# Optimization experiments

Hardware: AMD Instinct MI355X
Metric: run time of the kernel (lower is better)

## Reference

```python
import jax, jax.numpy as jnp
import numpy as np

N_MODEL = 10000
N_DATA = 552
DIST_SCALE = 1.0e5  # scales uniform [0,1) to realistic squared distances (meters^2)


def setup_inputs() -> dict:
    key = jax.random.key(0)
    k0, k1, k2 = jax.random.split(key, 3)
    distance_mesh = jax.random.uniform(k0, (N_MODEL, N_MODEL), dtype=jnp.float32) * DIST_SCALE
    F = jax.random.normal(k1, (N_DATA, N_MODEL), dtype=jnp.float32) * 0.01
    d_obs = jax.random.normal(k2, (N_DATA, 1), dtype=jnp.float32)
    data_std = 0.1
    data_cov = (data_std ** 2) * jnp.eye(N_DATA, dtype=jnp.float32)
    m0 = jnp.asarray(2200.0, dtype=jnp.float32)
    length_scale = jnp.asarray(100.0, dtype=jnp.float32)
    sigma = jnp.asarray(20.0, dtype=jnp.float32)
    return {
        "distance_mesh": distance_mesh,
        "F": F,
        "d_obs": d_obs,
        "data_cov": data_cov,
        "m0": m0,
        "length_scale": length_scale,
        "sigma": sigma,
    }


def reference(distance_mesh, F, d_obs, data_cov, m0, length_scale, sigma):
    n_model = distance_mesh.shape[0]
    # m_prior = m0 * ones([n_model, 1])
    m_prior = m0 * jnp.ones((n_model, 1), dtype=distance_mesh.dtype)
    # Squared-exponential covariance: sigma^2 * exp(-d / (2 l^2))  [n_model, n_model]
    K = jnp.exp(distance_mesh * (-1.0 / (2.0 * length_scale ** 2))) * (sigma ** 2)
    # pushforward covariance K @ F.T  [n_model, n_data]
    pushforward_cov = K @ F.T
    # data-space operator [n_data, n_data]
    inv_inversion_operator = data_cov + F @ pushforward_cov
    inversion_operator = jnp.linalg.inv(inv_inversion_operator)
    log_det = -jnp.linalg.slogdet(inversion_operator)[1]
    prior_misfit = d_obs - F @ m_prior  # [n_data, 1]
    tmp = inversion_operator @ prior_misfit  # [n_data, 1]
    m_posterior = m_prior + pushforward_cov @ tmp  # [n_model, 1]
    log_likelyhood = log_det + prior_misfit.T @ tmp  # [1, 1]
    return (log_likelyhood, m_posterior)
```

## Files before the change

kernel.cpp:

```cpp
#include <hip/hip_runtime.h>
#include <stdint.h>


#define NM 10000
#define ND 552
#define NDP 576
#define NKB 313
#define MT1 79
#define SPLITK 3
#define SPLITK2 6

typedef __attribute__((ext_vector_type(8))) short bf16x8;
typedef __attribute__((ext_vector_type(4))) float f32x4;

__device__ __forceinline__ unsigned short f2bf(float f){
  unsigned u = __float_as_uint(f);
  u += 0x7fffu + ((u >> 16) & 1u);
  return (unsigned short)(u >> 16);
}
__device__ __forceinline__ unsigned int pk2(unsigned short a, unsigned short b){
  return (unsigned int)a | ((unsigned int)b << 16);
}

__global__ void prep_bt(const float* __restrict__ F, unsigned short* __restrict__ Bt){
  int bid = blockIdx.x;
  int kb = bid % NKB, nb = bid / NKB;
  int t = threadIdx.x;
  int nl = t >> 2, q = t & 3;
  int gn = nb * 64 + nl;
  int k0 = kb * 32 + q * 8;
  float v[8];
  if (gn < ND && (k0 + 8) <= NM){
    const float* p = F + (size_t)gn * NM + k0;
    float4 a = *(const float4*)p;
    float4 b = *(const float4*)(p + 4);
    v[0]=a.x; v[1]=a.y; v[2]=a.z; v[3]=a.w; v[4]=b.x; v[5]=b.y; v[6]=b.z; v[7]=b.w;
  } else {
    #pragma unroll
    for (int i = 0; i < 8; ++i) v[i] = 0.f;
  }
  unsigned short u[8];
  #pragma unroll
  for (int i = 0; i < 8; ++i) u[i] = f2bf(v[i]);
  size_t cidx = ((size_t)kb * NDP + gn) * 4 + ((q + (gn >> 1)) & 3);
  uint4 w;
  w.x = pk2(u[0],u[1]); w.y = pk2(u[2],u[3]); w.z = pk2(u[4],u[5]); w.w = pk2(u[6],u[7]);
  *(uint4*)(Bt + cidx * 8) = w;
}

__global__ void rvec(const float* __restrict__ F, const float* __restrict__ dobs,
                     const float* __restrict__ m0p, float* __restrict__ r){
  __shared__ float red[256];
  int i = blockIdx.x;
  int t = threadIdx.x;
  float s = 0.f;
  if (i < ND){
    for (int k = t; k < NM; k += 256) s += F[(size_t)i * NM + k];
  }
  red[t] = s;
  __syncthreads();
  if (t < 64){
    float v = red[t] + red[t+64] + red[t+128] + red[t+192];
    #pragma unroll
    for (int off = 32; off; off >>= 1) v += __shfl_down(v, off);
    if (t == 0){
      if (i < ND) r[i] = dobs[i] - m0p[0] * v;
      else        r[i] = 0.f;
    }
  }
}

__global__ __launch_bounds__(512, 2) void gemm1(
    const float* __restrict__ dist, const unsigned short* __restrict__ Bt,
    float* __restrict__ P, const float* __restrict__ lsp, const float* __restrict__ sgp){
  __shared__ unsigned short Alds[2][128 * 40];
  __shared__ unsigned short Blds[2][NDP * 32];
  int bid = blockIdx.x;
  int mtile = bid % MT1, kc = bid / MT1;
  int kb0 = (kc == 0) ? 0 : (105 + 104 * (kc - 1));
  int kbe = kb0 + ((kc == 0) ? 105 : 104);
  int m0 = mtile * 128;
  float ls = lsp[0], sg = sgp[0];
  float ce = -0.72134752044f / (ls * ls);
  float s2 = sg * sg;
  int t = threadIdx.x, lane = t & 63, w = t >> 6;
  int wm = w & 1, wn = w >> 1;
  int c16 = lane & 15, q2 = lane >> 4;
  f32x4 acc[4][9];
  #pragma unroll
  for (int a = 0; a < 4; ++a)
    #pragma unroll
    for (int b = 0; b < 9; ++b) acc[a][b] = (f32x4){0.f, 0.f, 0.f, 0.f};

  int rr = t >> 2, qa = t & 3;
  const int arow = (wm * 64 + c16) * 40 + q2 * 8;
  int gm = m0 + rr;
  const float* arow_p = dist + (size_t)gm * NM;

  float av[8];
  uint4 bv[4];
  uint4 btl;
  bool aok = false;

#define G1_ISSUE(KB) { \
    int k0_ = (KB) * 32 + qa * 8; \
    aok = (gm < NM) && (k0_ + 8 <= NM); \
    if (aok){ \
      const float4* p_ = (const float4*)(arow_p + k0_); \
      float4 x_ = p_[0]; float4 y_ = p_[1]; \
      av[0]=x_.x; av[1]=x_.y; av[2]=x_.z; av[3]=x_.w; \
      av[4]=y_.x; av[5]=y_.y; av[6]=y_.z; av[7]=y_.w; \
    } \
    const uint4* bs_ = (const uint4*)Bt + (size_t)(KB) * NDP * 4; \
    bv[0] = bs_[t]; bv[1] = bs_[t + 512]; bv[2] = bs_[t + 1024]; bv[3] = bs_[t + 1536]; \
    if (t < 256) btl = bs_[t + 2048]; \
  }

#define G1_STORE(BUF) { \
    unsigned short u_[8]; \
    if (aok){ \
      _Pragma("unroll") \
      for (int i_ = 0; i_ < 8; ++i_) u_[i_] = f2bf(s2 * exp2f(av[i_] * ce)); \
    } else { \
      _Pragma("unroll") \
      for (int i_ = 0; i_ < 8; ++i_) u_[i_] = 0; \
    } \
    uint4 wv_; \
    wv_.x = pk2(u_[0],u_[1]); wv_.y = pk2(u_[2],u_[3]); \
    wv_.z = pk2(u_[4],u_[5]); wv_.w = pk2(u_[6],u_[7]); \
    *(uint4*)&Alds[BUF][rr * 40 + qa * 8] = wv_; \
    uint4* bd_ = (uint4*)Blds[BUF]; \
    bd_[t] = bv[0]; bd_[t + 512] = bv[1]; bd_[t + 1024] = bv[2]; bd_[t + 1536] = bv[3]; \
    if (t < 256) bd_[t + 2048] = btl; \
  }

  G1_ISSUE(kb0);
  G1_STORE(0);
  __syncthreads();

  for (int kb = kb0; kb < kbe; ++kb){
    int cur = (kb - kb0) & 1;
    if (kb + 1 < kbe) G1_ISSUE(kb + 1);
    bf16x8 af[4];
    #pragma unroll
    for (int mt = 0; mt < 4; ++mt)
      af[mt] = *(const bf16x8*)&Alds[cur][arow + mt * 16 * 40];
    #pragma unroll
    for (int nt = 0; nt < 9; ++nt){
      int n = wn * 144 + nt * 16 + c16;
      int cidx = n * 4 + ((q2 + (n >> 1)) & 3);
      bf16x8 bfv = *(const bf16x8*)&Blds[cur][cidx * 8];
      #pragma unroll
      for (int mt = 0; mt < 4; ++mt)
        acc[mt][nt] = __builtin_amdgcn_mfma_f32_16x16x32_bf16(af[mt], bfv, acc[mt][nt], 0, 0, 0);
    }
    if (kb + 1 < kbe) G1_STORE(cur ^ 1);
    __syncthreads();
  }
#undef G1_ISSUE
#undef G1_STORE

  #pragma unroll
  for (int mt = 0; mt < 4; ++mt)
    #pragma unroll
    for (int nt = 0; nt < 9; ++nt)
      #pragma unroll
      for (int e = 0; e < 4; ++e){
        int gmo = m0 + wm * 64 + mt * 16 + q2 * 4 + e;
        int gno = wn * 144 + nt * 16 + c16;
        if (gmo < NM) atomicAdd(&P[(size_t)gmo * NDP + gno], acc[mt][nt][e]);
      }
}

__global__ void conv_p(const float* __restrict__ P, unsigned short* __restrict__ Pb){
  int bid = blockIdx.x;
  int kb = bid % NKB, nb = bid / NKB;
  int t = threadIdx.x;
  int nl = t & 63, q = t >> 6;
  int gn = nb * 64 + nl;
  int k0 = kb * 32 + q * 8;
  unsigned short u[8];
  #pragma unroll
  for (int j = 0; j < 8; ++j){
    int k = k0 + j;
    float v = (k < NM) ? P[(size_t)k * NDP + gn] : 0.f;
    u[j] = f2bf(v);
  }
  size_t cidx = ((size_t)kb * NDP + gn) * 4 + ((q + (gn >> 1)) & 3);
  uint4 w;
  w.x = pk2(u[0],u[1]); w.y = pk2(u[2],u[3]); w.z = pk2(u[4],u[5]); w.w = pk2(u[6],u[7]);
  *(uint4*)(Pb + cidx * 8) = w;
}

__global__ void a_init(const float* __restrict__ dcov, float* __restrict__ A){
  int idx = blockIdx.x * 256 + threadIdx.x;
  if (idx >= NDP * NDP) return;
  int i = idx / NDP, j = idx % NDP;
  float v;
  if (i < ND && j < ND) v = dcov[i * ND + j];
  else v = (i == j) ? 1.f : 0.f;
  A[idx] = v;
}

__global__ __launch_bounds__(256) void gemm2(
    const unsigned short* __restrict__ Bt, const unsigned short* __restrict__ Pb,
    float* __restrict__ A){
  __shared__ unsigned short Fa[2][64 * 32];
  __shared__ unsigned short Pl[2][64 * 32];
  int bid = blockIdx.x;
  int tile = bid % 81, kc = bid / 81;
  int ti = tile / 9, tj = tile % 9;
  int i0 = ti * 64, j0 = tj * 64;
  int kb0 = (kc == 0) ? 0 : (53 + 52 * (kc - 1));
  int kbe = kb0 + ((kc == 0) ? 53 : 52);
  int t = threadIdx.x, lane = t & 63, w = t >> 6;
  int wm = w & 1, wn = w >> 1;
  int c16 = lane & 15, q2 = lane >> 4;
  f32x4 acc[2][2];
  #pragma unroll
  for (int a = 0; a < 2; ++a)
    #pragma unroll
    for (int b = 0; b < 2; ++b) acc[a][b] = (f32x4){0.f, 0.f, 0.f, 0.f};

  uint4 fv, pv;
  fv = ((const uint4*)Bt)[((size_t)kb0 * NDP + i0) * 4 + t];
  pv = ((const uint4*)Pb)[((size_t)kb0 * NDP + j0) * 4 + t];
  ((uint4*)Fa[0])[t] = fv;
  ((uint4*)Pl[0])[t] = pv;
  __syncthreads();

  for (int kb = kb0; kb < kbe; ++kb){
    int cur = (kb - kb0) & 1;
    if (kb + 1 < kbe){
      fv = ((const uint4*)Bt)[((size_t)(kb + 1) * NDP + i0) * 4 + t];
      pv = ((const uint4*)Pb)[((size_t)(kb + 1) * NDP + j0) * 4 + t];
    }
    bf16x8 af[2], bfv[2];
    #pragma unroll
    for (int mt = 0; mt < 2; ++mt){
      int il = wm * 32 + mt * 16 + c16;
      af[mt] = *(const bf16x8*)&Fa[cur][(il * 4 + ((q2 + (il >> 1)) & 3)) * 8];
    }
    #pragma unroll
    for (int nt = 0; nt < 2; ++nt){
      int jl = wn * 32 + nt * 16 + c16;
      bfv[nt] = *(const bf16x8*)&Pl[cur][(jl * 4 + ((q2 + (jl >> 1)) & 3)) * 8];
    }
    #pragma unroll
    for (int mt = 0; mt < 2; ++mt)
      #pragma unroll
      for (int nt = 0; nt < 2; ++nt)
        acc[mt][nt] = __builtin_amdgcn_mfma_f32_16x16x32_bf16(af[mt], bfv[nt], acc[mt][nt], 0, 0, 0);
    if (kb + 1 < kbe){
      ((uint4*)Fa[cur ^ 1])[t] = fv;
      ((uint4*)Pl[cur ^ 1])[t] = pv;
    }
    __syncthreads();
  }
  #pragma unroll
  for (int mt = 0; mt < 2; ++mt)
    #pragma unroll
    for (int nt = 0; nt < 2; ++nt)
      #pragma unroll
      for (int e = 0; e < 4; ++e){
        int gi = i0 + wm * 32 + mt * 16 + q2 * 4 + e;
        int gj = j0 + wn * 32 + nt * 16 + c16;
        atomicAdd(&A[(size_t)gi * NDP + gj], acc[mt][nt][e]);
      }
}

__global__ __launch_bounds__(256) void lu_trsm(float* __restrict__ A,
                                               float* __restrict__ D, int k0){
  __shared__ float Dg[64 * 65];
  __shared__ float Tg[64 * 65];
  int t = threadIdx.x;
  int nch = (NDP - k0 - 64) >> 6;
  int bid = blockIdx.x;
  bool writer = (bid == 2 * nch);
  bool isU = bid < nch;
  int ch = isU ? bid : bid - nch;
  int c0 = k0 + 64 + ch * 64;
  int rbase = isU ? k0 : c0;
  int cbase = isU ? c0 : k0;
  for (int fid = t; fid < 1024; fid += 256){
    int row = fid >> 4, c4 = (fid & 15) << 2;
    float4 v = *(const float4*)&A[(size_t)(k0 + row) * NDP + k0 + c4];
    Dg[row * 65 + c4 + 0] = v.x; Dg[row * 65 + c4 + 1] = v.y;
    Dg[row * 65 + c4 + 2] = v.z; Dg[row * 65 + c4 + 3] = v.w;
  }
  if (!writer){
    for (int fid = t; fid < 1024; fid += 256){
      int row = fid >> 4, c4 = (fid & 15) << 2;
      float4 v = *(const float4*)&A[(size_t)(rbase + row) * NDP + cbase + c4];
      Tg[row * 65 + c4 + 0] = v.x; Tg[row * 65 + c4 + 1] = v.y;
      Tg[row * 65 + c4 + 2] = v.z; Tg[row * 65 + c4 + 3] = v.w;
    }
  }
  __syncthreads();
  if (t < 64){
    int l = t;
    float rg[64];
    #pragma unroll
    for (int c = 0; c < 64; ++c) rg[c] = Dg[l * 65 + c];
    #pragma unroll
    for (int j = 0; j < 64; ++j){
      float piv = __shfl(rg[j], j);
      float lij = rg[j] / piv;
      float m = (l > j) ? 1.f : 0.f;
      float mlij = m * lij;
      #pragma unroll
      for (int c = j + 1; c < 64; ++c){
        float rjc = __shfl(rg[c], j);
        rg[c] -= mlij * rjc;
      }
      if (l > j) rg[j] = lij;
    }
    #pragma unroll
    for (int c = 0; c < 64; ++c) Dg[l * 65 + c] = rg[c];
  }
  __syncthreads();
  if (writer){
    float* dd = D + (size_t)(k0 >> 6) * 4096;
    for (int fid = t; fid < 1024; fid += 256){
      int row = fid >> 4, c4 = (fid & 15) << 2;
      float4 v;
      v.x = Dg[row * 65 + c4 + 0]; v.y = Dg[row * 65 + c4 + 1];
      v.z = Dg[row * 65 + c4 + 2]; v.w = Dg[row * 65 + c4 + 3];
      *(float4*)&dd[row * 64 + c4] = v;
    }
    return;
  }
  if (t < 64){
    if (isU){
      float x[64];
      #pragma unroll
      for (int i = 0; i < 64; ++i) x[i] = Tg[i * 65 + t];
      #pragma unroll
      for (int i = 0; i < 64; ++i){
        #pragma unroll
        for (int ii = i + 1; ii < 64; ++ii)
          x[ii] -= Dg[ii * 65 + i] * x[i];
      }
      #pragma unroll
      for (int i = 0; i < 64; ++i) Tg[i * 65 + t] = x[i];
    } else {
      float x[64];
      #pragma unroll
      for (int j = 0; j < 64; ++j) x[j] = Tg[t * 65 + j];
      #pragma unroll
      for (int j = 0; j < 64; ++j){
        x[j] /= Dg[j * 65 + j];
        #pragma unroll
        for (int jj = j + 1; jj < 64; ++jj)
          x[jj] -= x[j] * Dg[j * 65 + jj];
      }
      #pragma unroll
      for (int j = 0; j < 64; ++j) Tg[t * 65 + j] = x[j];
    }
  }
  __syncthreads();
  for (int fid = t; fid < 1024; fid += 256){
    int row = fid >> 4, c4 = (fid & 15) << 2;
    float4 v;
    v.x = Tg[row * 65 + c4 + 0]; v.y = Tg[row * 65 + c4 + 1];
    v.z = Tg[row * 65 + c4 + 2]; v.w = Tg[row * 65 + c4 + 3];
    *(float4*)&A[(size_t)(rbase + row) * NDP + cbase + c4] = v;
  }
}

__global__ __launch_bounds__(256) void lu_gemmk(float* __restrict__ A, int k0){
  __shared__ float Lt[32 * 65];
  __shared__ float Ut[64 * 33];
  int n2 = NDP - k0 - 64;
  int nb = n2 >> 5;
  int bx = blockIdx.x % nb, by = blockIdx.x / nb;
  int r0 = k0 + 64 + bx * 32, c0 = k0 + 64 + by * 32;
  int t = threadIdx.x;
  for (int idx = t; idx < 2048; idx += 256){
    int i = idx >> 6, kk = idx & 63;
    Lt[i * 65 + kk] = A[(size_t)(r0 + i) * NDP + k0 + kk];
  }
  for (int idx = t; idx < 2048; idx += 256){
    int kk = idx >> 5, j = idx & 31;
    Ut[kk * 33 + j] = A[(size_t)(k0 + kk) * NDP + c0 + j];
  }
  __syncthreads();
  int i = t >> 3, j4 = (t & 7) * 4;
  float acc[4] = {0.f, 0.f, 0.f, 0.f};
  for (int kk = 0; kk < 64; ++kk){
    float lv = Lt[i * 65 + kk];
    #pragma unroll
    for (int u = 0; u < 4; ++u) acc[u] += lv * Ut[kk * 33 + j4 + u];
  }
  float* dst = &A[(size_t)(r0 + i) * NDP + c0 + j4];
  #pragma unroll
  for (int u = 0; u < 4; ++u) dst[u] -= acc[u];
}

__global__ __launch_bounds__(576) void solve_ll(
    const float* __restrict__ A, const float* __restrict__ D,
    const float* __restrict__ r, float* __restrict__ tmp, float* __restrict__ out0){
  __shared__ float ys[NDP];
  __shared__ float red[16];
  int t = threadIdx.x;
  int w = t >> 6, l = t & 63;
  int i = t;
  float y = r[i];
  float rsave = y;
  float ldpart = 0.f;
  float row[64];

  for (int jb = 0; jb < 9; ++jb){
    if (w == jb){
      const float4* ap = (const float4*)(D + (size_t)jb * 4096 + (size_t)l * 64);
      #pragma unroll
      for (int q = 0; q < 16; ++q) ((float4*)row)[q] = ap[q];
    } else if (w > jb){
      const float4* ap = (const float4*)(A + (size_t)i * NDP + jb * 64);
      #pragma unroll
      for (int q = 0; q < 16; ++q) ((float4*)row)[q] = ap[q];
    }
    if (w == jb){
      #pragma unroll
      for (int j = 0; j < 64; ++j){
        float yj = __shfl(y, j);
        if (l > j) y -= row[j] * yj;
      }
      ys[i] = y;
    }
    __syncthreads();
    if (w > jb){
      #pragma unroll
      for (int j = 0; j < 64; ++j) y -= row[j] * ys[jb * 64 + j];
    }
  }
  __syncthreads();

  for (int jb = 8; jb >= 0; --jb){
    if (w == jb){
      const float4* ap = (const float4*)(D + (size_t)jb * 4096 + (size_t)l * 64);
      #pragma unroll
      for (int q = 0; q < 16; ++q) ((float4*)row)[q] = ap[q];
    } else if (w < jb){
      const float4* ap = (const float4*)(A + (size_t)i * NDP + jb * 64);
      #pragma unroll
      for (int q = 0; q < 16; ++q) ((float4*)row)[q] = ap[q];
    }
    if (w == jb){
      float dv = D[(size_t)jb * 4096 + (size_t)l * 64 + l];
      float dinv = 1.f / dv;
      ldpart = logf(fabsf(dv));
      #pragma unroll
      for (int j = 63; j >= 0; --j){
        float yj = __shfl(y, j) * __shfl(dinv, j);
        if (l == j) y = yj;
        if (l < j)  y -= row[j] * yj;
      }
      ys[i] = y;
    }
    __syncthreads();
    if (w < jb){
      #pragma unroll
      for (int j = 0; j < 64; ++j) y -= row[j] * ys[jb * 64 + j];
    }
  }

  tmp[i] = y;
  float contrib = ldpart + rsave * y;
  #pragma unroll
  for (int off = 32; off; off >>= 1) contrib += __shfl_down(contrib, off);
  if (l == 0) red[w] = contrib;
  __syncthreads();
  if (t == 0){
    float s = 0.f;
    #pragma unroll
    for (int k = 0; k < 9; ++k) s += red[k];
    out0[0] = s;
  }
}

__global__ void mpost(const float* __restrict__ P, const float* __restrict__ tmp,
                      const float* __restrict__ m0p, float* __restrict__ out1){
  int w = threadIdx.x >> 6, l = threadIdx.x & 63;
  int m = blockIdx.x * 4 + w;
  if (m >= NM) return;
  float s = 0.f;
  #pragma unroll
  for (int i = 0; i < 9; ++i){
    int n = i * 64 + l;
    s += P[(size_t)m * NDP + n] * tmp[n];
  }
  #pragma unroll
  for (int off = 32; off; off >>= 1) s += __shfl_down(s, off);
  if (l == 0) out1[m] = m0p[0] + s;
}

extern "C" void kernel_launch(void* const* d_in, const int* in_sizes, int n_in,
                              void* d_out, int out_size, void* d_ws, size_t ws_size,
                              hipStream_t stream){
  const float* dist = (const float*)d_in[0];
  const float* F    = (const float*)d_in[1];
  const float* dobs = (const float*)d_in[2];
  const float* dcov = (const float*)d_in[3];
  const float* m0p  = (const float*)d_in[4];
  const float* lsp  = (const float*)d_in[5];
  const float* sgp  = (const float*)d_in[6];
  float* out = (float*)d_out;
  char* ws = (char*)d_ws;

  unsigned short* Bt = (unsigned short*)(ws + 0);
  float*          P  = (float*)(ws + 11538432);
  unsigned short* Pb = (unsigned short*)(ws + 34578432);
  float*          A  = (float*)(ws + 46116864);
  float*          r  = (float*)(ws + 47443968);
  float*          tp = (float*)(ws + 47446272);
  float*          D  = (float*)(ws + 34578432);

  hipMemsetAsync(P, 0, (size_t)NM * NDP * sizeof(float), stream);
  prep_bt<<<NKB * 9, 256, 0, stream>>>(F, Bt);
  rvec<<<NDP, 256, 0, stream>>>(F, dobs, m0p, r);
  gemm1<<<MT1 * SPLITK, 512, 0, stream>>>(dist, Bt, P, lsp, sgp);
  conv_p<<<NKB * 9, 256, 0, stream>>>(P, Pb);
  a_init<<<(NDP * NDP) / 256, 256, 0, stream>>>(dcov, A);
  gemm2<<<81 * SPLITK2, 256, 0, stream>>>(Bt, Pb, A);
  for (int k = 0; k < 9; ++k){
    int nch = 8 - k;
    lu_trsm<<<2 * nch + 1, 256, 0, stream>>>(A, D, k * 64);
    if (k < 8){
      int nb = (NDP - k * 64 - 64) >> 5;
      lu_gemmk<<<nb * nb, 256, 0, stream>>>(A, k * 64);
    }
  }
  solve_ll<<<1, 576, 0, stream>>>(A, D, r, tp, out);
  mpost<<<2500, 256, 0, stream>>>(P, tp, m0p, out + 1);
}
```

Before: 1.518 ms.

## Drop LDS staging in gemm1, load operands directly to registers; fuse prep kernels

gemm1 now uses 64-row M tiles (157 tiles) and loads dist rows and the pre-swizzled bf16 F^T fragments straight from global memory into registers, double-buffered in two sets. This removes LDS staging and the per-step __syncthreads. Each wave reads its own B fragments, so B traffic from L2 rises, since the 576-wide B tile is no longer shared through LDS across waves. The prep_bt, rvec and a_init kernels are also merged into one launch with block-range dispatch, which saves two kernel launches.

```diff
diff --git a/kernel.cpp b/kernel.cpp
--- a/kernel.cpp
+++ b/kernel.cpp
@@ -6,9 +6,13 @@
 #define ND 552
 #define NDP 576
 #define NKB 313
-#define MT1 79
+#define MT1 157
 #define SPLITK 3
 #define SPLITK2 6
+
+#define PREP_BT_BLOCKS (NKB * 9)
+#define RVEC_BLOCKS    NDP
+#define AINIT_BLOCKS   ((NDP * NDP) / 256)
 
 typedef __attribute__((ext_vector_type(8))) short bf16x8;
 typedef __attribute__((ext_vector_type(4))) float f32x4;
@@ -22,50 +26,60 @@
   return (unsigned int)a | ((unsigned int)b << 16);
 }
 
-__global__ void prep_bt(const float* __restrict__ F, unsigned short* __restrict__ Bt){
-  int bid = blockIdx.x;
-  int kb = bid % NKB, nb = bid / NKB;
+__global__ void prep_fused(const float* __restrict__ F, const float* __restrict__ dobs,
+                           const float* __restrict__ m0p, const float* __restrict__ dcov,
+                           unsigned short* __restrict__ Bt, float* __restrict__ r,
+                           float* __restrict__ A){
+  __shared__ float red[256];
+  int b = blockIdx.x;
   int t = threadIdx.x;
-  int nl = t >> 2, q = t & 3;
-  int gn = nb * 64 + nl;
-  int k0 = kb * 32 + q * 8;
-  float v[8];
-  if (gn < ND && (k0 + 8) <= NM){
-    const float* p = F + (size_t)gn * NM + k0;
-    float4 a = *(const float4*)p;
-    float4 b = *(const float4*)(p + 4);
-    v[0]=a.x; v[1]=a.y; v[2]=a.z; v[3]=a.w; v[4]=b.x; v[5]=b.y; v[6]=b.z; v[7]=b.w;
+  if (b < PREP_BT_BLOCKS){
+    int kb = b % NKB, nb = b / NKB;
+    int nl = t >> 2, q = t & 3;
+    int gn = nb * 64 + nl;
+    int k0 = kb * 32 + q * 8;
+    float v[8];
+    if (gn < ND && (k0 + 8) <= NM){
+      const float* p = F + (size_t)gn * NM + k0;
+      float4 a = *(const float4*)p;
+      float4 bb = *(const float4*)(p + 4);
+      v[0]=a.x; v[1]=a.y; v[2]=a.z; v[3]=a.w; v[4]=bb.x; v[5]=bb.y; v[6]=bb.z; v[7]=bb.w;
+    } else {
+      #pragma unroll
+      for (int i = 0; i < 8; ++i) v[i] = 0.f;
+    }
+    unsigned short u[8];
+    #pragma unroll
+    for (int i = 0; i < 8; ++i) u[i] = f2bf(v[i]);
+    size_t cidx = ((size_t)kb * NDP + gn) * 4 + ((q + (gn >> 1)) & 3);
+    uint4 w;
+    w.x = pk2(u[0],u[1]); w.y = pk2(u[2],u[3]); w.z = pk2(u[4],u[5]); w.w = pk2(u[6],u[7]);
+    *(uint4*)(Bt + cidx * 8) = w;
+  } else if (b < PREP_BT_BLOCKS + RVEC_BLOCKS){
+    int i = b - PREP_BT_BLOCKS;
+    float s = 0.f;
+    if (i < ND){
+      for (int k = t; k < NM; k += 256) s += F[(size_t)i * NM + k];
+    }
+    red[t] = s;
+    __syncthreads();
+    if (t < 64){
+      float v = red[t] + red[t+64] + red[t+128] + red[t+192];
+      #pragma unroll
+      for (int off = 32; off; off >>= 1) v += __shfl_down(v, off);
+      if (t == 0){
+        if (i < ND) r[i] = dobs[i] - m0p[0] * v;
+        else        r[i] = 0.f;
+      }
+    }
   } else {
-    #pragma unroll
-    for (int i = 0; i < 8; ++i) v[i] = 0.f;
-  }
-  unsigned short u[8];
-  #pragma unroll
-  for (int i = 0; i < 8; ++i) u[i] = f2bf(v[i]);
-  size_t cidx = ((size_t)kb * NDP + gn) * 4 + ((q + (gn >> 1)) & 3);
-  uint4 w;
-  w.x = pk2(u[0],u[1]); w.y = pk2(u[2],u[3]); w.z = pk2(u[4],u[5]); w.w = pk2(u[6],u[7]);
-  *(uint4*)(Bt + cidx * 8) = w;
-}
-
-__global__ void rvec(const float* __restrict__ F, const float* __restrict__ dobs,
-                     const float* __restrict__ m0p, float* __restrict__ r){
-  __shared__ float red[256];
-  int i = blockIdx.x;
-  int t = threadIdx.x;
-  float s = 0.f;
-  if (i < ND){
-    for (int k = t; k < NM; k += 256) s += F[(size_t)i * NM + k];
-  }
-  red[t] = s;
-  __syncthreads();
-  if (t < 64){
-    float v = red[t] + red[t+64] + red[t+128] + red[t+192];
-    #pragma unroll
-    for (int off = 32; off; off >>= 1) v += __shfl_down(v, off);
-    if (t == 0){
-      if (i < ND) r[i] = dobs[i] - m0p[0] * v;
-      else        r[i] = 0.f;
+    int idx = (b - PREP_BT_BLOCKS - RVEC_BLOCKS) * 256 + t;
+    if (idx < NDP * NDP){
+      int i = idx / NDP, j = idx % NDP;
+      float v;
+      if (i < ND && j < ND) v = dcov[i * ND + j];
+      else v = (i == j) ? 1.f : 0.f;
+      A[idx] = v;
     }
   }
 }
@@ -73,100 +87,100 @@
 __global__ __launch_bounds__(512, 2) void gemm1(
     const float* __restrict__ dist, const unsigned short* __restrict__ Bt,
     float* __restrict__ P, const float* __restrict__ lsp, const float* __restrict__ sgp){
-  __shared__ unsigned short Alds[2][128 * 40];
-  __shared__ unsigned short Blds[2][NDP * 32];
   int bid = blockIdx.x;
   int mtile = bid % MT1, kc = bid / MT1;
   int kb0 = (kc == 0) ? 0 : (105 + 104 * (kc - 1));
   int kbe = kb0 + ((kc == 0) ? 105 : 104);
-  int m0 = mtile * 128;
+  int m0 = mtile * 64;
   float ls = lsp[0], sg = sgp[0];
   float ce = -0.72134752044f / (ls * ls);
   float s2 = sg * sg;
   int t = threadIdx.x, lane = t & 63, w = t >> 6;
   int wm = w & 1, wn = w >> 1;
   int c16 = lane & 15, q2 = lane >> 4;
-  f32x4 acc[4][9];
-  #pragma unroll
-  for (int a = 0; a < 4; ++a)
-    #pragma unroll
-    for (int b = 0; b < 9; ++b) acc[a][b] = (f32x4){0.f, 0.f, 0.f, 0.f};
-
-  int rr = t >> 2, qa = t & 3;
-  const int arow = (wm * 64 + c16) * 40 + q2 * 8;
-  int gm = m0 + rr;
-  const float* arow_p = dist + (size_t)gm * NM;
-
-  float av[8];
-  uint4 bv[4];
-  uint4 btl;
-  bool aok = false;
-
-#define G1_ISSUE(KB) { \
-    int k0_ = (KB) * 32 + qa * 8; \
-    aok = (gm < NM) && (k0_ + 8 <= NM); \
-    if (aok){ \
-      const float4* p_ = (const float4*)(arow_p + k0_); \
-      float4 x_ = p_[0]; float4 y_ = p_[1]; \
-      av[0]=x_.x; av[1]=x_.y; av[2]=x_.z; av[3]=x_.w; \
-      av[4]=y_.x; av[5]=y_.y; av[6]=y_.z; av[7]=y_.w; \
+
+  int r0 = m0 + wm * 32 + c16;
+  int r1 = r0 + 16;
+  const float* pa0 = dist + (size_t)(r0 < NM ? r0 : NM - 1) * NM;
+  const float* pa1 = dist + (size_t)(r1 < NM ? r1 : NM - 1) * NM;
+  int koff = q2 * 8;
+
+  const char* pbbase = (const char*)Bt;
+  int boff[9];
+  #pragma unroll
+  for (int nt = 0; nt < 9; ++nt){
+    int n = wn * 144 + nt * 16 + c16;
+    boff[nt] = (n * 4 + ((q2 + (n >> 1)) & 3)) * 16;
+  }
+
+  f32x4 acc[2][9];
+  #pragma unroll
+  for (int a = 0; a < 2; ++a)
+    #pragma unroll
+    for (int bq = 0; bq < 9; ++bq) acc[a][bq] = (f32x4){0.f, 0.f, 0.f, 0.f};
+
+  float4 avA[4], avB[4];
+  bf16x8 bfA[9], bfB[9];
+  bool okA = false, okB = false;
+
+#define G1_ISSUE(SET, KB) { \
+    int k0_ = (KB) * 32 + koff; \
+    ok##SET = (k0_ + 8 <= NM); \
+    if (ok##SET){ \
+      const float4* a0_ = (const float4*)(pa0 + k0_); \
+      const float4* a1_ = (const float4*)(pa1 + k0_); \
+      av##SET[0] = a0_[0]; av##SET[1] = a0_[1]; \
+      av##SET[2] = a1_[0]; av##SET[3] = a1_[1]; \
     } \
-    const uint4* bs_ = (const uint4*)Bt + (size_t)(KB) * NDP * 4; \
-    bv[0] = bs_[t]; bv[1] = bs_[t + 512]; bv[2] = bs_[t + 1024]; bv[3] = bs_[t + 1536]; \
-    if (t < 256) btl = bs_[t + 2048]; \
-  }
-
-#define G1_STORE(BUF) { \
-    unsigned short u_[8]; \
-    if (aok){ \
+    const char* bs_ = pbbase + (size_t)(KB) * (NDP * 32 * 2); \
+    _Pragma("unroll") \
+    for (int nt_ = 0; nt_ < 9; ++nt_) \
+      bf##SET[nt_] = *(const bf16x8*)(bs_ + boff[nt_]); \
+  }
+
+#define G1_CONSUME(SET) { \
+    unsigned short u_[16]; \
+    if (ok##SET){ \
+      float vv_[16]; \
+      vv_[0]=av##SET[0].x; vv_[1]=av##SET[0].y; vv_[2]=av##SET[0].z; vv_[3]=av##SET[0].w; \
+      vv_[4]=av##SET[1].x; vv_[5]=av##SET[1].y; vv_[6]=av##SET[1].z; vv_[7]=av##SET[1].w; \
+      vv_[8]=av##SET[2].x; vv_[9]=av##SET[2].y; vv_[10]=av##SET[2].z; vv_[11]=av##SET[2].w; \
+      vv_[12]=av##SET[3].x; vv_[13]=av##SET[3].y; vv_[14]=av##SET[3].z; vv_[15]=av##SET[3].w; \
       _Pragma("unroll") \
-      for (int i_ = 0; i_ < 8; ++i_) u_[i_] = f2bf(s2 * exp2f(av[i_] * ce)); \
+      for (int i_ = 0; i_ < 16; ++i_) u_[i_] = f2bf(s2 * exp2f(vv_[i_] * ce)); \
     } else { \
       _Pragma("unroll") \
-      for (int i_ = 0; i_ < 8; ++i_) u_[i_] = 0; \
+      for (int i_ = 0; i_ < 16; ++i_) u_[i_] = 0; \
     } \
-    uint4 wv_; \
-    wv_.x = pk2(u_[0],u_[1]); wv_.y = pk2(u_[2],u_[3]); \
-    wv_.z = pk2(u_[4],u_[5]); wv_.w = pk2(u_[6],u_[7]); \
-    *(uint4*)&Alds[BUF][rr * 40 + qa * 8] = wv_; \
-    uint4* bd_ = (uint4*)Blds[BUF]; \
-    bd_[t] = bv[0]; bd_[t + 512] = bv[1]; bd_[t + 1024] = bv[2]; bd_[t + 1536] = bv[3]; \
-    if (t < 256) bd_[t + 2048] = btl; \
-  }
-
-  G1_ISSUE(kb0);
-  G1_STORE(0);
-  __syncthreads();
-
-  for (int kb = kb0; kb < kbe; ++kb){
-    int cur = (kb - kb0) & 1;
-    if (kb + 1 < kbe) G1_ISSUE(kb + 1);
-    bf16x8 af[4];
-    #pragma unroll
-    for (int mt = 0; mt < 4; ++mt)
-      af[mt] = *(const bf16x8*)&Alds[cur][arow + mt * 16 * 40];
-    #pragma unroll
-    for (int nt = 0; nt < 9; ++nt){
-      int n = wn * 144 + nt * 16 + c16;
-      int cidx = n * 4 + ((q2 + (n >> 1)) & 3);
-      bf16x8 bfv = *(const bf16x8*)&Blds[cur][cidx * 8];
-      #pragma unroll
-      for (int mt = 0; mt < 4; ++mt)
-        acc[mt][nt] = __builtin_amdgcn_mfma_f32_16x16x32_bf16(af[mt], bfv, acc[mt][nt], 0, 0, 0);
-    }
-    if (kb + 1 < kbe) G1_STORE(cur ^ 1);
-    __syncthreads();
+    bf16x8 af0_, af1_; \
+    _Pragma("unroll") \
+    for (int i_ = 0; i_ < 8; ++i_){ af0_[i_] = (short)u_[i_]; af1_[i_] = (short)u_[i_ + 8]; } \
+    _Pragma("unroll") \
+    for (int nt_ = 0; nt_ < 9; ++nt_){ \
+      acc[0][nt_] = __builtin_amdgcn_mfma_f32_16x16x32_bf16(af0_, bf##SET[nt_], acc[0][nt_], 0, 0, 0); \
+      acc[1][nt_] = __builtin_amdgcn_mfma_f32_16x16x32_bf16(af1_, bf##SET[nt_], acc[1][nt_], 0, 0, 0); \
+    } \
+  }
+
+  G1_ISSUE(A, kb0);
+  for (int kb = kb0; kb < kbe; kb += 2){
+    if (kb + 1 < kbe) G1_ISSUE(B, kb + 1);
+    G1_CONSUME(A);
+    if (kb + 1 < kbe){
+      if (kb + 2 < kbe) G1_ISSUE(A, kb + 2);
+      G1_CONSUME(B);
+    }
   }
 #undef G1_ISSUE
-#undef G1_STORE
-
-  #pragma unroll
-  for (int mt = 0; mt < 4; ++mt)
+#undef G1_CONSUME
+
+  #pragma unroll
+  for (int mt = 0; mt < 2; ++mt)
     #pragma unroll
     for (int nt = 0; nt < 9; ++nt)
       #pragma unroll
       for (int e = 0; e < 4; ++e){
-        int gmo = m0 + wm * 64 + mt * 16 + q2 * 4 + e;
+        int gmo = m0 + wm * 32 + mt * 16 + q2 * 4 + e;
         int gno = wn * 144 + nt * 16 + c16;
         if (gmo < NM) atomicAdd(&P[(size_t)gmo * NDP + gno], acc[mt][nt][e]);
       }
@@ -190,16 +204,6 @@
   uint4 w;
   w.x = pk2(u[0],u[1]); w.y = pk2(u[2],u[3]); w.z = pk2(u[4],u[5]); w.w = pk2(u[6],u[7]);
   *(uint4*)(Pb + cidx * 8) = w;
-}
-
-__global__ void a_init(const float* __restrict__ dcov, float* __restrict__ A){
-  int idx = blockIdx.x * 256 + threadIdx.x;
-  if (idx >= NDP * NDP) return;
-  int i = idx / NDP, j = idx % NDP;
-  float v;
-  if (i < ND && j < ND) v = dcov[i * ND + j];
-  else v = (i == j) ? 1.f : 0.f;
-  A[idx] = v;
 }
 
 __global__ __launch_bounds__(256) void gemm2(
@@ -517,11 +521,10 @@
   float*          D  = (float*)(ws + 34578432);
 
   hipMemsetAsync(P, 0, (size_t)NM * NDP * sizeof(float), stream);
-  prep_bt<<<NKB * 9, 256, 0, stream>>>(F, Bt);
-  rvec<<<NDP, 256, 0, stream>>>(F, dobs, m0p, r);
+  prep_fused<<<PREP_BT_BLOCKS + RVEC_BLOCKS + AINIT_BLOCKS, 256, 0, stream>>>(
+      F, dobs, m0p, dcov, Bt, r, A);
   gemm1<<<MT1 * SPLITK, 512, 0, stream>>>(dist, Bt, P, lsp, sgp);
   conv_p<<<NKB * 9, 256, 0, stream>>>(P, Pb);
-  a_init<<<(NDP * NDP) / 256, 256, 0, stream>>>(dcov, A);
   gemm2<<<81 * SPLITK2, 256, 0, stream>>>(Bt, Pb, A);
   for (int k = 0; k < 9; ++k){
     int nch = 8 - k;
```

Measured after the change: 1.387 ms. -8.6%, faster.
